# Kernel tuning notes

Hardware: AMD Instinct MI355X
Metric: run time of the kernel (lower is better)

Reference implementation:

```python
import jax, jax.numpy as jnp
import numpy as np

B, KB, SEQ, HID = 8, 16, 512, 768  # batch, two_times_batch, max_length, hidden
NEG_INF = float('-inf')


def _l2_normalize(x, eps=1e-12):
    # torch F.normalize: x / max(||x||_2, eps)
    n = jnp.sqrt(jnp.sum(x * x, axis=-1, keepdims=True))
    return x / jnp.maximum(n, eps)


def setup_inputs() -> dict:
    key = jax.random.key(0)
    k1, k2, k3, k4 = jax.random.split(key, 4)
    return {
        'query_embs': jax.random.normal(k1, (B, SEQ, HID), dtype=jnp.float32),
        'key_embs': jax.random.normal(k2, (KB, SEQ, HID), dtype=jnp.float32),
        'alpha_raw': jnp.float32(0.1),  # learnable scalar, cfg.model.alpha init
        'q_mask': jax.random.randint(k3, (B, SEQ), 0, 2, dtype=jnp.int32),
        'k_mask': jax.random.randint(k4, (KB, SEQ), 0, 2, dtype=jnp.int32),
    }


def reference(query_embs, key_embs, alpha_raw, q_mask, k_mask):
    # cfg: distance_weightning='exp', use_softmax=True, gumbel_temp=None
    qn = _l2_normalize(query_embs)          # [B, S, H]
    kn = _l2_normalize(key_embs)            # [KB, T, H]

    # cosine similarity: [B, KB, S, T]
    sim = jnp.einsum('ish,jth->ijst', qn, kn)

    # exp distance weighting, alpha = leaky_relu(alpha_raw)
    alpha = jax.nn.leaky_relu(alpha_raw)
    pos = jnp.arange(SEQ, dtype=jnp.float32)
    distance = jnp.abs(pos[:, None] - pos[None, :])        # [S, T]
    sim = sim * jnp.exp(-alpha * distance)

    valid = (q_mask[:, None, :, None] != 0) & (k_mask[None, :, None, :] != 0)
    logits = jnp.where(valid, sim, NEG_INF)

    p = jax.nn.softmax(logits, axis=-1)                    # [B, KB, S, T]
    p = jnp.nan_to_num(p, nan=0.0)

    # aggregate normalized keys under attention, dot with queries
    aggregated = jnp.einsum('ijst,jth->ijsh', p, kn)       # [B, KB, S, H]
    scores = jnp.einsum('ish,ijsh->ijs', qn, aggregated)   # [B, KB, S]
    scores = scores * q_mask[:, None, :].astype(scores.dtype)
    return scores.sum(axis=-1)                             # [B, KB]
```

## Files before the change

kernel.cpp:

```cpp
#include <hip/hip_runtime.h>
#include <stdint.h>

#define B_   8
#define KB_  16
#define SEQ_ 512
#define HID_ 768

#define NKB  (HID_ / 32)
#define QRB  (B_  * SEQ_ / 16)
#define KRB  (KB_ * SEQ_ / 16)

typedef __attribute__((ext_vector_type(4))) _Float16 half4;
typedef __attribute__((ext_vector_type(8))) _Float16 half8;
typedef __attribute__((ext_vector_type(4))) float    floatx4;

#define GLOBAL_AS __attribute__((address_space(1)))
#define LDS_AS    __attribute__((address_space(3)))

static __device__ __forceinline__ void async_tile16(const _Float16* g, _Float16* l)
{
    __builtin_amdgcn_global_load_lds((const GLOBAL_AS uint32_t*)g,
                                     (LDS_AS uint32_t*)l, 16, 0, 0);
}

#define LP 776

__global__ __launch_bounds__(256)
void prep_tile(const float* __restrict__ Q, const float* __restrict__ K,
               _Float16* __restrict__ Qt, _Float16* __restrict__ Kt)
{
    const int rb = blockIdx.x;
    const float* src;
    _Float16*    dst;
    if (rb < QRB) { src = Q + (size_t)rb * 16 * HID_;          dst = Qt + (size_t)rb * NKB * 512; }
    else          { src = K + (size_t)(rb - QRB) * 16 * HID_;  dst = Kt + (size_t)(rb - QRB) * NKB * 512; }

    __shared__ _Float16 Ls[16 * LP];
    const int wave = threadIdx.x >> 6;
    const int lane = threadIdx.x & 63;

#pragma unroll
    for (int rr = 0; rr < 4; ++rr) {
        int row = wave * 4 + rr;
        const float* s = src + (size_t)row * HID_;
        float4 v[3];
        float ss = 0.f;
#pragma unroll
        for (int it = 0; it < 3; ++it) {
            v[it] = *(const float4*)(s + lane * 4 + it * 256);
            ss += v[it].x * v[it].x + v[it].y * v[it].y + v[it].z * v[it].z + v[it].w * v[it].w;
        }
#pragma unroll
        for (int m = 1; m < 64; m <<= 1) ss += __shfl_xor(ss, m, 64);
        float sc = 1.0f / fmaxf(sqrtf(ss), 1e-12f);
#pragma unroll
        for (int it = 0; it < 3; ++it) {
            half4 h = { (_Float16)(v[it].x * sc), (_Float16)(v[it].y * sc),
                        (_Float16)(v[it].z * sc), (_Float16)(v[it].w * sc) };
            *(half4*)(Ls + row * LP + lane * 4 + it * 256) = h;
        }
    }
    __syncthreads();

#pragma unroll
    for (int rep = 0; rep < 6; ++rep) {
        int slot = rep * 256 + threadIdx.x;
        int kb   = slot >> 6;
        int ln   = slot & 63;
        int row  = ln & 15;
        int ko   = kb * 32 + (ln >> 4) * 8;
        half8 h = *(const half8*)(Ls + row * LP + ko);
        *(half8*)(dst + (size_t)kb * 512 + (size_t)ln * 8) = h;
    }
}

__global__ __launch_bounds__(256, 4)
void li_part(const _Float16* __restrict__ Qt, const _Float16* __restrict__ Kt,
             const float* __restrict__ alpha_p, const int* __restrict__ kmask,
             float* __restrict__ Pbuf)
{
    const int st = blockIdx.x >> 2;
    const int tb = blockIdx.x & 3;
    const int j  = blockIdx.y;
    const int i  = blockIdx.z;

    const int tid  = threadIdx.x;
    const int lane = tid & 63;
    const int wave = tid >> 6;
    const int quad = lane >> 4;
    const int l16  = lane & 15;
    const int wr   = wave >> 1;
    const int wc   = wave & 1;

    __shared__ __align__(16) _Float16 smem[2 * 16 * 512];
    __shared__ float lred[2][128], nred[2][128];

    const float araw  = *alpha_p;
    const float alpha = araw >= 0.f ? araw : 0.01f * araw;

    const int qbase = i * 32 + st * 8;
    const int kbase = j * 32 + tb * 8;

    const _Float16* gsrc[4];
    _Float16*       ldst0[4];
#pragma unroll
    for (int q = 0; q < 4; ++q) {
        int t   = wave * 4 + q;
        int rbg = (t < 8) ? (qbase + t) : (kbase + (t - 8));
        const _Float16* base = (t < 8) ? Qt : Kt;
        gsrc[q]  = base + (size_t)rbg * NKB * 512 + (size_t)lane * 8;
        ldst0[q] = &smem[t * 512];
    }

    floatx4 acc[4][4];
#pragma unroll
    for (int rt = 0; rt < 4; ++rt)
#pragma unroll
        for (int ct = 0; ct < 4; ++ct)
            acc[rt][ct] = (floatx4){0.f, 0.f, 0.f, 0.f};

#pragma unroll
    for (int q = 0; q < 4; ++q)
        async_tile16(gsrc[q], ldst0[q]);

    for (int kb = 0; kb < NKB; ++kb) {
        const int b = kb & 1;
        __syncthreads();
        if (kb + 1 < NKB) {
#pragma unroll
            for (int q = 0; q < 4; ++q)
                async_tile16(gsrc[q] + (size_t)(kb + 1) * 512, ldst0[q] + (b ^ 1) * 16 * 512);
        }
        const _Float16* Qs = &smem[b * 16 * 512];
        const _Float16* Ks = Qs + 8 * 512;
        half8 af[4], bf[4];
#pragma unroll
        for (int rt = 0; rt < 4; ++rt)
            af[rt] = *(const half8*)(Qs + (wr * 4 + rt) * 512 + lane * 8);
#pragma unroll
        for (int ct = 0; ct < 4; ++ct)
            bf[ct] = *(const half8*)(Ks + (wc * 4 + ct) * 512 + lane * 8);
#pragma unroll
        for (int rt = 0; rt < 4; ++rt)
#pragma unroll
            for (int ct = 0; ct < 4; ++ct)
                acc[rt][ct] = __builtin_amdgcn_mfma_f32_16x16x32_f16(af[rt], bf[ct], acc[rt][ct], 0, 0, 0);
    }

    const int* km = kmask + j * SEQ_ + tb * 128;
    int kmv[4]; float tgf[4];
#pragma unroll
    for (int ct = 0; ct < 4; ++ct) {
        int t_loc = wc * 64 + ct * 16 + l16;
        kmv[ct] = km[t_loc];
        tgf[ct] = (float)(tb * 128 + t_loc);
    }
#pragma unroll
    for (int rt = 0; rt < 4; ++rt) {
#pragma unroll
        for (int r = 0; r < 4; ++r) {
            float sgf = (float)(st * 128 + wr * 64 + rt * 16 + quad * 4 + r);
            float ps = 0.f, ns = 0.f;
#pragma unroll
            for (int ct = 0; ct < 4; ++ct) {
                float cv = acc[rt][ct][r];
                float e  = kmv[ct] ? __expf(cv * __expf(-alpha * fabsf(sgf - tgf[ct]))) : 0.f;
                ps += e;
                ns += e * cv;
            }
#pragma unroll
            for (int msk = 1; msk < 16; msk <<= 1) {
                ps += __shfl_xor(ps, msk, 64);
                ns += __shfl_xor(ns, msk, 64);
            }
            if (l16 == 0) {
                int rloc = wr * 64 + rt * 16 + quad * 4 + r;
                lred[wc][rloc] = ps;
                nred[wc][rloc] = ns;
            }
        }
    }
    __syncthreads();

    if (tid < 128) {
        float l = lred[0][tid] + lred[1][tid];
        float n = nred[0][tid] + nred[1][tid];
        size_t base = (((size_t)(i * KB_ + j) * SEQ_) + st * 128 + tid) * 8 + tb * 2;
        Pbuf[base]     = l;
        Pbuf[base + 1] = n;
    }
}

__global__ __launch_bounds__(256)
void li_reduce(const float* __restrict__ Pbuf, const int* __restrict__ qmask,
               float* __restrict__ out)
{
    const int ij = blockIdx.x;
    const int i  = ij >> 4;
    const int tid = threadIdx.x;
    __shared__ float red[4];

    float sum = 0.f;
#pragma unroll
    for (int rep = 0; rep < 2; ++rep) {
        int s = tid + rep * 256;
        const float4* p = (const float4*)(Pbuf + ((size_t)ij * SEQ_ + s) * 8);
        float4 a = p[0], b = p[1];
        float l = a.x + a.z + b.x + b.z;
        float n = a.y + a.w + b.y + b.w;
        float sc = (l > 0.f) ? n / l : 0.f;
        if (qmask[i * SEQ_ + s] == 0) sc = 0.f;
        sum += sc;
    }
#pragma unroll
    for (int m = 1; m < 64; m <<= 1) sum += __shfl_xor(sum, m, 64);
    if ((tid & 63) == 0) red[tid >> 6] = sum;
    __syncthreads();
    if (tid == 0) out[ij] = red[0] + red[1] + red[2] + red[3];
}

extern "C" void kernel_launch(void* const* d_in, const int* in_sizes, int n_in,
                              void* d_out, int out_size, void* d_ws, size_t ws_size,
                              hipStream_t stream)
{
    const float* Q       = (const float*)d_in[0];
    const float* K       = (const float*)d_in[1];
    const float* alpha_p = (const float*)d_in[2];
    const int*   qmask   = (const int*)d_in[3];
    const int*   kmask   = (const int*)d_in[4];
    float*       out     = (float*)d_out;

    char* ws = (char*)d_ws;
    _Float16* Qt   = (_Float16*)ws;
    _Float16* Kt   = (_Float16*)(ws + (size_t)B_ * SEQ_ * HID_ * 2);
    float*    Pbuf = (float*)   (ws + (size_t)(B_ + KB_) * SEQ_ * HID_ * 2);

    prep_tile<<<QRB + KRB, 256, 0, stream>>>(Q, K, Qt, Kt);

    dim3 grid(16, KB_, B_);
    li_part<<<grid, 256, 0, stream>>>(Qt, Kt, alpha_p, kmask, Pbuf);

    li_reduce<<<B_ * KB_, 256, 0, stream>>>(Pbuf, qmask, out);
}
```

Before: 145.8 us.

## Compact valid query/key rows via mask prefix scan and skip masked tiles

A new scan kernel prefix-sums the query and key masks, so only valid rows are written, compacted, into row-major fp16 buffers, along with their original position indices. The attention kernel then skips 128x128 tiles that lie entirely beyond the valid counts and uses the stored original indices for the distance weighting. With random masks about half the rows are valid, so roughly three quarters of the tile work can be skipped. The cost is an extra launch, padding writes, and a layout change: the per-lane global_load_lds now gathers 16-byte pieces from separate rows with a stride of HID instead of reading contiguous pre-tiled blocks.

```diff
diff --git a/kernel.cpp b/kernel.cpp
--- a/kernel.cpp
+++ b/kernel.cpp
@@ -23,25 +23,80 @@
                                      (LDS_AS uint32_t*)l, 16, 0, 0);
 }
 
-#define LP 776
+__global__ __launch_bounds__(512)
+void scan_mask(const int* __restrict__ qmask, const int* __restrict__ kmask,
+               int* __restrict__ pos_of, float* __restrict__ oidxf,
+               int* __restrict__ nvalid,
+               _Float16* __restrict__ Qc, _Float16* __restrict__ Kc)
+{
+    const int b   = blockIdx.x;
+    const int tid = threadIdx.x;
+    const int* m  = (b < 8) ? (qmask + b * SEQ_) : (kmask + (b - 8) * SEQ_);
+    const int lane = tid & 63, wave = tid >> 6;
+
+    int v = (m[tid] != 0) ? 1 : 0;
+    int x = v;
+#pragma unroll
+    for (int off = 1; off < 64; off <<= 1) {
+        int y = __shfl_up(x, off, 64);
+        if (lane >= off) x += y;
+    }
+    __shared__ int wsum[8];
+    __shared__ int nv_s;
+    if (lane == 63) wsum[wave] = x;
+    __syncthreads();
+    int base = 0;
+#pragma unroll
+    for (int w = 0; w < 8; ++w) base += (w < wave) ? wsum[w] : 0;
+    int incl = base + x;
+    int pos  = incl - v;
+    pos_of[b * SEQ_ + tid] = v ? pos : -1;
+    if (v) oidxf[b * SEQ_ + pos] = (float)tid;
+    if (tid == 511) nv_s = incl;
+    __syncthreads();
+    int nv = nv_s;
+    if (tid == 0) nvalid[b] = nv;
+    if (tid >= nv) oidxf[b * SEQ_ + tid] = 0.f;
+
+    int lim = (nv + 127) & ~127;
+    if (lim > SEQ_) lim = SEQ_;
+    _Float16* dstb = (b < 8) ? (Qc + (size_t)b * SEQ_ * HID_)
+                             : (Kc + (size_t)(b - 8) * SEQ_ * HID_);
+    for (int p = nv + tid; p < lim; p += 512) {
+        _Float16* d = dstb + (size_t)p * HID_;
+        half8 z = {0, 0, 0, 0, 0, 0, 0, 0};
+#pragma unroll
+        for (int c = 0; c < HID_ / 8; ++c) *(half8*)(d + c * 8) = z;
+    }
+}
 
 __global__ __launch_bounds__(256)
-void prep_tile(const float* __restrict__ Q, const float* __restrict__ K,
-               _Float16* __restrict__ Qt, _Float16* __restrict__ Kt)
+void prep_norm(const float* __restrict__ Q, const float* __restrict__ K,
+               const int* __restrict__ pos_of,
+               _Float16* __restrict__ Qc, _Float16* __restrict__ Kc)
 {
     const int rb = blockIdx.x;
-    const float* src;
-    _Float16*    dst;
-    if (rb < QRB) { src = Q + (size_t)rb * 16 * HID_;          dst = Qt + (size_t)rb * NKB * 512; }
-    else          { src = K + (size_t)(rb - QRB) * 16 * HID_;  dst = Kt + (size_t)(rb - QRB) * NKB * 512; }
-
-    __shared__ _Float16 Ls[16 * LP];
+    const float* src; _Float16* dstb; const int* pf;
+    if (rb < QRB) {
+        int i = rb >> 5;
+        src  = Q + (size_t)rb * 16 * HID_;
+        dstb = Qc + (size_t)i * SEQ_ * HID_;
+        pf   = pos_of + i * SEQ_ + (rb & 31) * 16;
+    } else {
+        int rk = rb - QRB;
+        int j  = rk >> 5;
+        src  = K + (size_t)rk * 16 * HID_;
+        dstb = Kc + (size_t)j * SEQ_ * HID_;
+        pf   = pos_of + (8 + j) * SEQ_ + (rk & 31) * 16;
+    }
     const int wave = threadIdx.x >> 6;
     const int lane = threadIdx.x & 63;
 
 #pragma unroll
     for (int rr = 0; rr < 4; ++rr) {
         int row = wave * 4 + rr;
+        int pos = pf[row];
+        if (pos < 0) continue;
         const float* s = src + (size_t)row * HID_;
         float4 v[3];
         float ss = 0.f;
@@ -53,31 +108,20 @@
 #pragma unroll
         for (int m = 1; m < 64; m <<= 1) ss += __shfl_xor(ss, m, 64);
         float sc = 1.0f / fmaxf(sqrtf(ss), 1e-12f);
+        _Float16* d = dstb + (size_t)pos * HID_;
 #pragma unroll
         for (int it = 0; it < 3; ++it) {
             half4 h = { (_Float16)(v[it].x * sc), (_Float16)(v[it].y * sc),
                         (_Float16)(v[it].z * sc), (_Float16)(v[it].w * sc) };
-            *(half4*)(Ls + row * LP + lane * 4 + it * 256) = h;
-        }
-    }
-    __syncthreads();
-
-#pragma unroll
-    for (int rep = 0; rep < 6; ++rep) {
-        int slot = rep * 256 + threadIdx.x;
-        int kb   = slot >> 6;
-        int ln   = slot & 63;
-        int row  = ln & 15;
-        int ko   = kb * 32 + (ln >> 4) * 8;
-        half8 h = *(const half8*)(Ls + row * LP + ko);
-        *(half8*)(dst + (size_t)kb * 512 + (size_t)ln * 8) = h;
+            *(half4*)(d + lane * 4 + it * 256) = h;
+        }
     }
 }
 
 __global__ __launch_bounds__(256, 4)
-void li_part(const _Float16* __restrict__ Qt, const _Float16* __restrict__ Kt,
-             const float* __restrict__ alpha_p, const int* __restrict__ kmask,
-             float* __restrict__ Pbuf)
+void li_part(const _Float16* __restrict__ Qc, const _Float16* __restrict__ Kc,
+             const float* __restrict__ alpha_p, const int* __restrict__ nvalid,
+             const float* __restrict__ oidxf, float* __restrict__ Pbuf)
 {
     const int st = blockIdx.x >> 2;
     const int tb = blockIdx.x & 3;
@@ -92,23 +136,36 @@
     const int wr   = wave >> 1;
     const int wc   = wave & 1;
 
+    const int nvq = nvalid[i];
+    const int nvk = nvalid[8 + j];
+    const int stiles = (nvq + 127) >> 7;
+    const int ttiles = (nvk + 127) >> 7;
+
+    const size_t pbase0 = (((size_t)(i * KB_ + j) * SEQ_) + st * 128) * 8 + tb * 2;
+    if (st >= stiles || tb >= ttiles) {
+        if (tid < 128) {
+            Pbuf[pbase0 + (size_t)tid * 8]     = 0.f;
+            Pbuf[pbase0 + (size_t)tid * 8 + 1] = 0.f;
+        }
+        return;
+    }
+
     __shared__ __align__(16) _Float16 smem[2 * 16 * 512];
     __shared__ float lred[2][128], nred[2][128];
 
     const float araw  = *alpha_p;
     const float alpha = araw >= 0.f ? araw : 0.01f * araw;
 
-    const int qbase = i * 32 + st * 8;
-    const int kbase = j * 32 + tb * 8;
-
     const _Float16* gsrc[4];
     _Float16*       ldst0[4];
 #pragma unroll
     for (int q = 0; q < 4; ++q) {
-        int t   = wave * 4 + q;
-        int rbg = (t < 8) ? (qbase + t) : (kbase + (t - 8));
-        const _Float16* base = (t < 8) ? Qt : Kt;
-        gsrc[q]  = base + (size_t)rbg * NKB * 512 + (size_t)lane * 8;
+        int t = wave * 4 + q;
+        size_t row;
+        const _Float16* basep;
+        if (t < 8) { row = (size_t)i * SEQ_ + st * 128 + t * 16 + (lane & 15);       basep = Qc; }
+        else       { row = (size_t)j * SEQ_ + tb * 128 + (t - 8) * 16 + (lane & 15); basep = Kc; }
+        gsrc[q]  = basep + row * HID_ + (lane >> 4) * 8;
         ldst0[q] = &smem[t * 512];
     }
 
@@ -129,7 +186,7 @@
         if (kb + 1 < NKB) {
 #pragma unroll
             for (int q = 0; q < 4; ++q)
-                async_tile16(gsrc[q] + (size_t)(kb + 1) * 512, ldst0[q] + (b ^ 1) * 16 * 512);
+                async_tile16(gsrc[q] + (size_t)(kb + 1) * 32, ldst0[q] + (b ^ 1) * 16 * 512);
         }
         const _Float16* Qs = &smem[b * 16 * 512];
         const _Float16* Ks = Qs + 8 * 512;
@@ -147,19 +204,21 @@
                 acc[rt][ct] = __builtin_amdgcn_mfma_f32_16x16x32_f16(af[rt], bf[ct], acc[rt][ct], 0, 0, 0);
     }
 
-    const int* km = kmask + j * SEQ_ + tb * 128;
+    const float* tgfp = oidxf + (8 + j) * SEQ_ + tb * 128;
+    const float* sgfp = oidxf + i * SEQ_ + st * 128;
     int kmv[4]; float tgf[4];
 #pragma unroll
     for (int ct = 0; ct < 4; ++ct) {
         int t_loc = wc * 64 + ct * 16 + l16;
-        kmv[ct] = km[t_loc];
-        tgf[ct] = (float)(tb * 128 + t_loc);
+        kmv[ct] = (tb * 128 + t_loc) < nvk;
+        tgf[ct] = tgfp[t_loc];
     }
 #pragma unroll
     for (int rt = 0; rt < 4; ++rt) {
 #pragma unroll
         for (int r = 0; r < 4; ++r) {
-            float sgf = (float)(st * 128 + wr * 64 + rt * 16 + quad * 4 + r);
+            int rloc = wr * 64 + rt * 16 + quad * 4 + r;
+            float sgf = sgfp[rloc];
             float ps = 0.f, ns = 0.f;
 #pragma unroll
             for (int ct = 0; ct < 4; ++ct) {
@@ -174,29 +233,24 @@
                 ns += __shfl_xor(ns, msk, 64);
             }
             if (l16 == 0) {
-                int rloc = wr * 64 + rt * 16 + quad * 4 + r;
-                lred[wc][rloc] = ps;
-                nred[wc][rloc] = ns;
+                int valid_row = (st * 128 + rloc) < nvq;
+                lred[wc][rloc] = valid_row ? ps : 0.f;
+                nred[wc][rloc] = valid_row ? ns : 0.f;
             }
         }
     }
     __syncthreads();
 
     if (tid < 128) {
-        float l = lred[0][tid] + lred[1][tid];
-        float n = nred[0][tid] + nred[1][tid];
-        size_t base = (((size_t)(i * KB_ + j) * SEQ_) + st * 128 + tid) * 8 + tb * 2;
-        Pbuf[base]     = l;
-        Pbuf[base + 1] = n;
+        Pbuf[pbase0 + (size_t)tid * 8]     = lred[0][tid] + lred[1][tid];
+        Pbuf[pbase0 + (size_t)tid * 8 + 1] = nred[0][tid] + nred[1][tid];
     }
 }
 
 __global__ __launch_bounds__(256)
-void li_reduce(const float* __restrict__ Pbuf, const int* __restrict__ qmask,
-               float* __restrict__ out)
-{
-    const int ij = blockIdx.x;
-    const int i  = ij >> 4;
+void li_reduce(const float* __restrict__ Pbuf, float* __restrict__ out)
+{
+    const int ij  = blockIdx.x;
     const int tid = threadIdx.x;
     __shared__ float red[4];
 
@@ -208,9 +262,7 @@
         float4 a = p[0], b = p[1];
         float l = a.x + a.z + b.x + b.z;
         float n = a.y + a.w + b.y + b.w;
-        float sc = (l > 0.f) ? n / l : 0.f;
-        if (qmask[i * SEQ_ + s] == 0) sc = 0.f;
-        sum += sc;
+        sum += (l > 0.f) ? n / l : 0.f;
     }
 #pragma unroll
     for (int m = 1; m < 64; m <<= 1) sum += __shfl_xor(sum, m, 64);
@@ -231,14 +283,21 @@
     float*       out     = (float*)d_out;
 
     char* ws = (char*)d_ws;
-    _Float16* Qt   = (_Float16*)ws;
-    _Float16* Kt   = (_Float16*)(ws + (size_t)B_ * SEQ_ * HID_ * 2);
-    float*    Pbuf = (float*)   (ws + (size_t)(B_ + KB_) * SEQ_ * HID_ * 2);
-
-    prep_tile<<<QRB + KRB, 256, 0, stream>>>(Q, K, Qt, Kt);
+    _Float16* Qc    = (_Float16*)ws;
+    _Float16* Kc    = (_Float16*)(ws + (size_t)B_ * SEQ_ * HID_ * 2);
+    float*    Pbuf  = (float*)   (ws + (size_t)(B_ + KB_) * SEQ_ * HID_ * 2);
+    char*     ws2   = ws + (size_t)(B_ + KB_) * SEQ_ * HID_ * 2
+                         + (size_t)B_ * KB_ * SEQ_ * 8 * sizeof(float);
+    int*      pos_of = (int*)ws2;
+    float*    oidxf  = (float*)(ws2 + 24 * SEQ_ * 4);
+    int*      nvalid = (int*)(ws2 + 2 * 24 * SEQ_ * 4);
+
+    scan_mask<<<24, 512, 0, stream>>>(qmask, kmask, pos_of, oidxf, nvalid, Qc, Kc);
+
+    prep_norm<<<QRB + KRB, 256, 0, stream>>>(Q, K, pos_of, Qc, Kc);
 
     dim3 grid(16, KB_, B_);
-    li_part<<<grid, 256, 0, stream>>>(Qt, Kt, alpha_p, kmask, Pbuf);
-
-    li_reduce<<<B_ * KB_, 256, 0, stream>>>(Pbuf, qmask, out);
-}
+    li_part<<<grid, 256, 0, stream>>>(Qc, Kc, alpha_p, nvalid, oidxf, Pbuf);
+
+    li_reduce<<<B_ * KB_, 256, 0, stream>>>(Pbuf, out);
+}
```

Result: slower. 199.5 us (+36.8%).
